# Kernel tuning notes

Hardware: AMD Instinct MI355X
Metric: run time of the kernel (lower is better)

The kernel has to match this reference:

```python
import jax, jax.numpy as jnp
import numpy as np

B = 131072          # number of pooled samples per feature
T = 1048576         # total jagged lookup values per feature
D = 64              # embedding dim
INPUT_HASH = 4000   # raw id space (input_hash_size)
ZCH_0 = 16          # table_0 zch_size
ZCH_1 = 32          # table_1 zch_size


def setup_inputs() -> dict:
    key = jax.random.key(0)
    k1, k2, k3, k4, k5, k6 = jax.random.split(key, 6)
    values_0 = jax.random.randint(k1, (T,), 0, INPUT_HASH, dtype=jnp.int64)
    segment_ids_0 = jnp.sort(jax.random.randint(k2, (T,), 0, B, dtype=jnp.int64))
    values_1 = jax.random.randint(k3, (T,), 0, INPUT_HASH, dtype=jnp.int64)
    segment_ids_1 = jnp.sort(jax.random.randint(k4, (T,), 0, B, dtype=jnp.int64))
    emb_0 = jax.random.normal(k5, (ZCH_0, D), dtype=jnp.float32)
    emb_1 = jax.random.normal(k6, (ZCH_1, D), dtype=jnp.float32)
    return {
        "values_0": values_0, "segment_ids_0": segment_ids_0,
        "values_1": values_1, "segment_ids_1": segment_ids_1,
        "emb_0": emb_0, "emb_1": emb_1,
    }


def _pooled_lookup(values, segment_ids, table, zch_size):
    # managed-collision mod-hash remap into the small zch id space
    remapped = jnp.mod(values, zch_size)
    # gather rows then sum-pool per sample (EmbeddingBag sum pooling)
    rows = jnp.take(table, remapped, axis=0)          # [T, D]
    pooled = jax.ops.segment_sum(rows, segment_ids, num_segments=B)  # [B, D]
    return pooled


def reference(values_0, segment_ids_0, values_1, segment_ids_1, emb_0, emb_1):
    p0 = _pooled_lookup(values_0, segment_ids_0, emb_0, ZCH_0)
    p1 = _pooled_lookup(values_1, segment_ids_1, emb_1, ZCH_1)
    pred = jnp.concatenate([p0, p1], axis=1)          # [B, 2*D]
    loss = jnp.mean(pred)
    return loss
```

## Files before the change

kernel.cpp:

```cpp
#include <hip/hip_runtime.h>


#define T_LEN   1048576
#define D_DIM   64
#define ZCH0    16
#define ZCH1    32
#define NB      256
#define NT      256

__global__ __launch_bounds__(NT) void sparse_pooled_mean_kernel(
    const int*   __restrict__ v0,
    const int*   __restrict__ v1,
    const float* __restrict__ emb0,
    const float* __restrict__ emb1,
    float*       __restrict__ out)
{
    __shared__ float rs[ZCH0 + ZCH1];
    __shared__ float red[NT / 64];

    const int tid = threadIdx.x;

    if (tid < ZCH0 + ZCH1) {
        const float4* row = (tid < ZCH0)
            ? (const float4*)(emb0 + tid * D_DIM)
            : (const float4*)(emb1 + (tid - ZCH0) * D_DIM);
        float s = 0.f;
        #pragma unroll
        for (int i = 0; i < D_DIM / 4; ++i) {
            float4 q = row[i];
            s += (q.x + q.y) + (q.z + q.w);
        }
        rs[tid] = s;
    }
    __syncthreads();

    const int4* p0 = (const int4*)v0;
    const int4* p1 = (const int4*)v1;
    const int n4 = T_LEN / 4;

    float acc = 0.f;
    for (int idx = blockIdx.x * NT + tid; idx < n4; idx += NB * NT) {
        int4 a = p0[idx];
        int4 b = p1[idx];
        acc += rs[a.x & (ZCH0 - 1)] + rs[a.y & (ZCH0 - 1)]
             + rs[a.z & (ZCH0 - 1)] + rs[a.w & (ZCH0 - 1)];
        acc += rs[ZCH0 + (b.x & (ZCH1 - 1))] + rs[ZCH0 + (b.y & (ZCH1 - 1))]
             + rs[ZCH0 + (b.z & (ZCH1 - 1))] + rs[ZCH0 + (b.w & (ZCH1 - 1))];
    }

    #pragma unroll
    for (int off = 32; off > 0; off >>= 1)
        acc += __shfl_down(acc, off, 64);

    const int lane = tid & 63;
    const int wave = tid >> 6;
    if (lane == 0) red[wave] = acc;
    __syncthreads();

    if (tid == 0) {
        float s = (red[0] + red[1]) + (red[2] + red[3]);
        atomicAdd(out, s * (1.0f / 16777216.0f));
    }
}

extern "C" void kernel_launch(void* const* d_in, const int* in_sizes, int n_in,
                              void* d_out, int out_size, void* d_ws, size_t ws_size,
                              hipStream_t stream) {
    const int*   v0   = (const int*)d_in[0];
    const int*   v1   = (const int*)d_in[2];
    const float* emb0 = (const float*)d_in[4];
    const float* emb1 = (const float*)d_in[5];
    float* out = (float*)d_out;

    hipMemsetAsync(out, 0, sizeof(float), stream);
    sparse_pooled_mean_kernel<<<NB, NT, 0, stream>>>(v0, v1, emb0, emb1, out);
}
```

Before: 75.33 us.

## Prefetch all index loads upfront and replace atomic+memset with two-stage reduction

The grid-stride loop is replaced by a fixed, fully unrolled set of four int4 loads per input array, all issued before any compute, so more memory requests are in flight per thread. The memset plus per-block atomicAdd is replaced by a per-block partial write to workspace and a second tiny kernel that reduces the 256 partials. This removes a memset launch and atomic contention but adds a second kernel launch, and it hardcodes that T_LEN/4 equals exactly K_ITERS*NB*NT.

New measurement: 73.69 us. 1.02x faster.

```diff
diff --git a/kernel.cpp b/kernel.cpp
--- a/kernel.cpp
+++ b/kernel.cpp
@@ -7,13 +7,14 @@
 #define ZCH1    32
 #define NB      256
 #define NT      256
+#define K_ITERS 4
 
-__global__ __launch_bounds__(NT) void sparse_pooled_mean_kernel(
+__global__ __launch_bounds__(NT) void partial_sum_kernel(
     const int*   __restrict__ v0,
     const int*   __restrict__ v1,
     const float* __restrict__ emb0,
     const float* __restrict__ emb1,
-    float*       __restrict__ out)
+    float*       __restrict__ partial)
 {
     __shared__ float rs[ZCH0 + ZCH1];
     __shared__ float red[NT / 64];
@@ -36,31 +37,47 @@
 
     const int4* p0 = (const int4*)v0;
     const int4* p1 = (const int4*)v1;
-    const int n4 = T_LEN / 4;
+    const int base = blockIdx.x * NT + tid;
+
+    int4 a[K_ITERS], b[K_ITERS];
+    #pragma unroll
+    for (int k = 0; k < K_ITERS; ++k) {
+        a[k] = p0[base + k * (NB * NT)];
+        b[k] = p1[base + k * (NB * NT)];
+    }
 
     float acc = 0.f;
-    for (int idx = blockIdx.x * NT + tid; idx < n4; idx += NB * NT) {
-        int4 a = p0[idx];
-        int4 b = p1[idx];
-        acc += rs[a.x & (ZCH0 - 1)] + rs[a.y & (ZCH0 - 1)]
-             + rs[a.z & (ZCH0 - 1)] + rs[a.w & (ZCH0 - 1)];
-        acc += rs[ZCH0 + (b.x & (ZCH1 - 1))] + rs[ZCH0 + (b.y & (ZCH1 - 1))]
-             + rs[ZCH0 + (b.z & (ZCH1 - 1))] + rs[ZCH0 + (b.w & (ZCH1 - 1))];
+    #pragma unroll
+    for (int k = 0; k < K_ITERS; ++k) {
+        acc += rs[a[k].x & (ZCH0 - 1)] + rs[a[k].y & (ZCH0 - 1)]
+             + rs[a[k].z & (ZCH0 - 1)] + rs[a[k].w & (ZCH0 - 1)];
+        acc += rs[ZCH0 + (b[k].x & (ZCH1 - 1))] + rs[ZCH0 + (b[k].y & (ZCH1 - 1))]
+             + rs[ZCH0 + (b[k].z & (ZCH1 - 1))] + rs[ZCH0 + (b[k].w & (ZCH1 - 1))];
     }
 
     #pragma unroll
     for (int off = 32; off > 0; off >>= 1)
         acc += __shfl_down(acc, off, 64);
 
-    const int lane = tid & 63;
-    const int wave = tid >> 6;
-    if (lane == 0) red[wave] = acc;
+    if ((tid & 63) == 0) red[tid >> 6] = acc;
     __syncthreads();
 
-    if (tid == 0) {
-        float s = (red[0] + red[1]) + (red[2] + red[3]);
-        atomicAdd(out, s * (1.0f / 16777216.0f));
-    }
+    if (tid == 0)
+        partial[blockIdx.x] = (red[0] + red[1]) + (red[2] + red[3]);
+}
+
+__global__ __launch_bounds__(64) void final_reduce_kernel(
+    const float* __restrict__ partial,
+    float*       __restrict__ out)
+{
+    const int t = threadIdx.x;
+    float4 q = ((const float4*)partial)[t];
+    float acc = (q.x + q.y) + (q.z + q.w);
+    #pragma unroll
+    for (int off = 32; off > 0; off >>= 1)
+        acc += __shfl_down(acc, off, 64);
+    if (t == 0)
+        out[0] = acc * (1.0f / 16777216.0f);
 }
 
 extern "C" void kernel_launch(void* const* d_in, const int* in_sizes, int n_in,
@@ -70,8 +87,9 @@
     const int*   v1   = (const int*)d_in[2];
     const float* emb0 = (const float*)d_in[4];
     const float* emb1 = (const float*)d_in[5];
-    float* out = (float*)d_out;
+    float* partial = (float*)d_ws;
+    float* out     = (float*)d_out;
 
-    hipMemsetAsync(out, 0, sizeof(float), stream);
-    sparse_pooled_mean_kernel<<<NB, NT, 0, stream>>>(v0, v1, emb0, emb1, out);
+    partial_sum_kernel<<<NB, NT, 0, stream>>>(v0, v1, emb0, emb1, partial);
+    final_reduce_kernel<<<1, 64, 0, stream>>>(partial, out);
 }
```
